# Optimization experiments

Hardware: AMD Instinct MI355X
Metric: run time of the kernel (lower is better)

Reference implementation:

```python
import jax, jax.numpy as jnp
import numpy as np

K = 5  # neighbors per node


def build_knn_adjacency(x, k=K):
    # x: (B, N, D) -> adj: (B, N, N)
    B, N, D = x.shape
    x_norm = x / jnp.clip(jnp.linalg.norm(x, axis=-1, keepdims=True), 1e-12)
    sim = jnp.einsum('bnd,bmd->bnm', x_norm, x_norm)  # (B, N, N)
    eye = jnp.eye(N, dtype=bool)
    sim = jnp.where(eye[None], jnp.asarray(-1.0, sim.dtype), sim)
    _, knn_idx = jax.lax.top_k(sim, k)  # (B, N, k)
    b_ix = jnp.arange(B)[:, None, None]
    i_ix = jnp.arange(N)[None, :, None]
    adj = jnp.zeros((B, N, N), dtype=x.dtype).at[b_ix, i_ix, knn_idx].set(1.0)
    adj = adj + jnp.eye(N, dtype=x.dtype)[None]
    return adj


def gcn_layer(x, adj, W, b):
    # deg-normalized aggregation then linear (torch Linear: x @ W.T + b)
    deg = adj.sum(axis=-1, keepdims=True)
    adj_norm = adj / jnp.clip(deg, 1.0)
    out = jnp.einsum('bnm,bmd->bnd', adj_norm, x)
    return out @ W.T + b


def setup_inputs() -> dict:
    key = jax.random.key(0)
    k1, k2, k3, k4, k5 = jax.random.split(key, 5)
    B, N, D, H = 32, 1024, 128, 128
    scale = 1.0 / np.sqrt(D)
    return {
        'x': jax.random.normal(k1, (B, N, D), dtype=jnp.float32),
        'W1': jax.random.normal(k2, (H, D), dtype=jnp.float32) * scale,
        'b1': jax.random.normal(k3, (H,), dtype=jnp.float32) * 0.01,
        'W2': jax.random.normal(k4, (H, H), dtype=jnp.float32) * scale,
        'b2': jax.random.normal(k5, (H,), dtype=jnp.float32) * 0.01,
    }


def reference(x, W1, b1, W2, b2):
    adj = build_knn_adjacency(x, k=K)
    h = x + jax.nn.relu(gcn_layer(x, adj, W1, b1))
    h = h + jax.nn.relu(gcn_layer(h, adj, W2, b2))
    return h  # pool='none' -> (B, N, hidden_dim)
```

## Files before the change

kernel.cpp:

```cpp
#include <hip/hip_runtime.h>
#include <float.h>
#include <math.h>

#define BB 32
#define NN 1024
#define DD 128
#define KK 5

typedef __attribute__((ext_vector_type(8))) short bf16x8;
typedef __attribute__((ext_vector_type(4))) float f32x4;

__device__ __forceinline__ unsigned short f2bf(float f) {
    unsigned int u = __float_as_uint(f);
    return (unsigned short)((u + 0x7FFFu + ((u >> 16) & 1u)) >> 16);
}
__device__ __forceinline__ float bf2f(unsigned short h) {
    return __uint_as_float(((unsigned int)h) << 16);
}

__device__ __forceinline__ void split2(const float4& a0, const float4& a1,
                                       bf16x8& hi, bf16x8& lo) {
    float v[8] = {a0.x, a0.y, a0.z, a0.w, a1.x, a1.y, a1.z, a1.w};
#pragma unroll
    for (int j = 0; j < 8; ++j) {
        unsigned short hb = f2bf(v[j]);
        float r = v[j] - bf2f(hb);
        unsigned short mb = f2bf(r);
        hi[j] = (short)hb;
        lo[j] = (short)mb;
    }
}

__global__ __launch_bounds__(256) void k_norm(const float* __restrict__ x,
                                              unsigned short* __restrict__ ph,
                                              unsigned short* __restrict__ pm,
                                              unsigned short* __restrict__ pl) {
    int row  = blockIdx.x * 4 + (threadIdx.x >> 6);
    int lane = threadIdx.x & 63;
    float2 v = *reinterpret_cast<const float2*>(x + (size_t)row * DD + lane * 2);
    float ss = v.x * v.x + v.y * v.y;
#pragma unroll
    for (int o = 32; o >= 1; o >>= 1) ss += __shfl_xor(ss, o);
    float inv = 1.0f / fmaxf(sqrtf(ss), 1e-12f);
    float y0 = v.x * inv, y1 = v.y * inv;

    unsigned short h0 = f2bf(y0);             float r0 = y0 - bf2f(h0);
    unsigned short m0 = f2bf(r0);             float s0 = r0 - bf2f(m0);
    unsigned short l0 = f2bf(s0);
    unsigned short h1 = f2bf(y1);             float r1 = y1 - bf2f(h1);
    unsigned short m1 = f2bf(r1);             float s1 = r1 - bf2f(m1);
    unsigned short l1 = f2bf(s1);

    size_t o = (size_t)row * DD + lane * 2;
    *reinterpret_cast<unsigned int*>(ph + o) = (unsigned int)h0 | ((unsigned int)h1 << 16);
    *reinterpret_cast<unsigned int*>(pm + o) = (unsigned int)m0 | ((unsigned int)m1 << 16);
    *reinterpret_cast<unsigned int*>(pl + o) = (unsigned int)l0 | ((unsigned int)l1 << 16);
}

union SMem {
    struct {
        unsigned short Ah[128][40], Am[128][40], Al[128][40];
        unsigned short Bh[128][40], Bm[128][40], Bl[128][40];
    } s;
    float q[4][32][68];
};

__device__ __forceinline__ void stage_plane(const unsigned short* __restrict__ g,
                                            unsigned short (*s)[40], int tid,
                                            size_t rowbase, int c) {
#pragma unroll
    for (int hh = 0; hh < 2; ++hh) {
        int u = tid + (hh << 8);
        int row = u >> 2, qq = u & 3;
        const float4 v = *reinterpret_cast<const float4*>(
            g + (rowbase + row) * DD + (c << 5) + (qq << 3));
        *reinterpret_cast<float4*>(&s[row][qq << 3]) = v;
    }
}

__global__ __launch_bounds__(256, 2) void k_sim(const unsigned short* __restrict__ ph,
                                                const unsigned short* __restrict__ pm,
                                                const unsigned short* __restrict__ pl,
                                                float* __restrict__ sim) {
    int bid = blockIdx.x;
    int lb  = (bid & 7) * 144 + (bid >> 3);
    int bl  = lb / 36;
    int p   = lb - bl * 36;
    int ti = 0;
    while (p >= 8 - ti) { p -= 8 - ti; ++ti; }
    int tj = ti + p;
    int R  = ti << 7, Cc = tj << 7;

    __shared__ SMem sm;

    int tid  = threadIdx.x;
    int wv   = tid >> 6;
    int lane = tid & 63;
    int wr = (wv >> 1) << 6;
    int wc = (wv & 1) << 6;
    int lg = lane >> 4, fr = lane & 15;

    size_t base = (size_t)bl * NN;
    size_t rbA = base + R, rbB = base + Cc;

    f32x4 acc[4][4];
#pragma unroll
    for (int i = 0; i < 4; ++i)
#pragma unroll
        for (int j = 0; j < 4; ++j) acc[i][j] = (f32x4){0.f, 0.f, 0.f, 0.f};

    int kk = lg << 3;

    for (int c = 0; c < 4; ++c) {
        if (c) __syncthreads();
        stage_plane(ph, sm.s.Ah, tid, rbA, c);
        stage_plane(pm, sm.s.Am, tid, rbA, c);
        stage_plane(pl, sm.s.Al, tid, rbA, c);
        stage_plane(ph, sm.s.Bh, tid, rbB, c);
        stage_plane(pm, sm.s.Bm, tid, rbB, c);
        stage_plane(pl, sm.s.Bl, tid, rbB, c);
        __syncthreads();

        bf16x8 bh[4], bm[4], blo[4];
#pragma unroll
        for (int cp = 0; cp < 4; ++cp) {
            int rb = wc + cp * 16 + fr;
            bh[cp]  = *reinterpret_cast<const bf16x8*>(&sm.s.Bh[rb][kk]);
            bm[cp]  = *reinterpret_cast<const bf16x8*>(&sm.s.Bm[rb][kk]);
            blo[cp] = *reinterpret_cast<const bf16x8*>(&sm.s.Bl[rb][kk]);
        }
#pragma unroll
        for (int rp = 0; rp < 4; ++rp) {
            int ra = wr + rp * 16 + fr;
            bf16x8 ah = *reinterpret_cast<const bf16x8*>(&sm.s.Ah[ra][kk]);
            bf16x8 am = *reinterpret_cast<const bf16x8*>(&sm.s.Am[ra][kk]);
            bf16x8 al = *reinterpret_cast<const bf16x8*>(&sm.s.Al[ra][kk]);
#pragma unroll
            for (int cp = 0; cp < 4; ++cp) {
                f32x4 cacc = acc[rp][cp];
                cacc = __builtin_amdgcn_mfma_f32_16x16x32_bf16(ah, bh[cp],  cacc, 0, 0, 0);
                cacc = __builtin_amdgcn_mfma_f32_16x16x32_bf16(ah, bm[cp],  cacc, 0, 0, 0);
                cacc = __builtin_amdgcn_mfma_f32_16x16x32_bf16(am, bh[cp],  cacc, 0, 0, 0);
                cacc = __builtin_amdgcn_mfma_f32_16x16x32_bf16(ah, blo[cp], cacc, 0, 0, 0);
                cacc = __builtin_amdgcn_mfma_f32_16x16x32_bf16(al, bh[cp],  cacc, 0, 0, 0);
                cacc = __builtin_amdgcn_mfma_f32_16x16x32_bf16(am, bm[cp],  cacc, 0, 0, 0);
                acc[rp][cp] = cacc;
            }
        }
    }

    __syncthreads();
    float (*q)[68] = sm.q[wv];
    float* Cb = sim + base * NN;

    if (ti != tj) {
#pragma unroll
        for (int hp = 0; hp < 2; ++hp) {
#pragma unroll
            for (int rp = 0; rp < 4; ++rp)
#pragma unroll
                for (int cpl = 0; cpl < 2; ++cpl) {
                    const f32x4 a = acc[rp][2 * hp + cpl];
                    *reinterpret_cast<float4*>(&q[cpl * 16 + fr][rp * 16 + lg * 4]) =
                        make_float4(a[0], a[1], a[2], a[3]);
                }
#pragma unroll
            for (int it = 0; it < 8; ++it) {
                int lcol = lg + 4 * it;
                const float4 v = *reinterpret_cast<const float4*>(&q[lcol][fr * 4]);
                *reinterpret_cast<float4*>(
                    &Cb[(size_t)(Cc + wc + 32 * hp + lcol) * NN + R + wr + fr * 4]) = v;
            }
        }
    }
#pragma unroll
    for (int hr = 0; hr < 2; ++hr) {
#pragma unroll
        for (int rpl = 0; rpl < 2; ++rpl)
#pragma unroll
            for (int cp = 0; cp < 4; ++cp)
#pragma unroll
                for (int reg = 0; reg < 4; ++reg)
                    q[rpl * 16 + lg * 4 + reg][cp * 16 + fr] = acc[2 * hr + rpl][cp][reg];
#pragma unroll
        for (int it = 0; it < 8; ++it) {
            int lrow = lg + 4 * it;
            const float4 v = *reinterpret_cast<const float4*>(&q[lrow][fr * 4]);
            *reinterpret_cast<float4*>(
                &Cb[(size_t)(R + wr + 32 * hr + lrow) * NN + Cc + wc + fr * 4]) = v;
        }
    }
}

__global__ __launch_bounds__(256) void k_topk(const float* __restrict__ sim,
                                              int* __restrict__ idx) {
    int lrow = blockIdx.x * 4 + (threadIdx.x >> 6);
    int lane = threadIdx.x & 63;
    const float* sr = sim + (size_t)lrow * NN;
    int i = lrow & (NN - 1);

    float v[16];
#pragma unroll
    for (int q = 0; q < 4; ++q) {
        float4 f = *reinterpret_cast<const float4*>(sr + lane * 16 + q * 4);
        v[q * 4 + 0] = f.x; v[q * 4 + 1] = f.y; v[q * 4 + 2] = f.z; v[q * 4 + 3] = f.w;
    }
    if ((i >> 4) == lane) {
        int s = i & 15;
#pragma unroll
        for (int j = 0; j < 16; ++j) if (j == s) v[j] = -FLT_MAX;
    }
    int* op = idx + (size_t)lrow * KK;
#pragma unroll
    for (int t = 0; t < KK; ++t) {
        float bv = v[0]; int bj = 0;
#pragma unroll
        for (int j = 1; j < 16; ++j) if (v[j] > bv) { bv = v[j]; bj = j; }
        int bm = (lane << 4) + bj;
#pragma unroll
        for (int o = 1; o < 64; o <<= 1) {
            float ov = __shfl_xor(bv, o);
            int   om = __shfl_xor(bm, o);
            if (ov > bv || (ov == bv && om < bm)) { bv = ov; bm = om; }
        }
        if ((bm >> 4) == lane) {
            int s = bm & 15;
#pragma unroll
            for (int j = 0; j < 16; ++j) if (j == s) v[j] = -FLT_MAX;
        }
        if (lane == 0) op[t] = bm;
    }
}

__global__ __launch_bounds__(256, 3) void k_gcn(const float* __restrict__ h,
                                                const int* __restrict__ idx,
                                                const float* __restrict__ W,
                                                const float* __restrict__ bias,
                                                const float* __restrict__ res,
                                                float* __restrict__ out) {
    int rt = blockIdx.x << 6;
    __shared__ float As[64][132];
    int tid = threadIdx.x;

    {
        int row = tid >> 2, fq = tid & 3;
        int grow = rt + row;
        const int* ip = idx + (size_t)grow * KK;
        const float* hb = h + (((size_t)grow >> 10) << 10) * DD;
        const float* hs = h + (size_t)grow * DD;
        int n0 = ip[0], n1 = ip[1], n2 = ip[2], n3 = ip[3], n4 = ip[4];
        const float* p0 = hb + (size_t)n0 * DD;
        const float* p1 = hb + (size_t)n1 * DD;
        const float* p2 = hb + (size_t)n2 * DD;
        const float* p3 = hb + (size_t)n3 * DD;
        const float* p4 = hb + (size_t)n4 * DD;
        const float cc = 1.0f / 6.0f;
#pragma unroll
        for (int rep = 0; rep < 8; ++rep) {
            int c = rep * 16 + fq * 4;
            float4 v  = *reinterpret_cast<const float4*>(hs + c);
            float4 u0 = *reinterpret_cast<const float4*>(p0 + c);
            float4 u1 = *reinterpret_cast<const float4*>(p1 + c);
            float4 u2 = *reinterpret_cast<const float4*>(p2 + c);
            float4 u3 = *reinterpret_cast<const float4*>(p3 + c);
            float4 u4 = *reinterpret_cast<const float4*>(p4 + c);
            v.x = (v.x + u0.x + u1.x + u2.x + u3.x + u4.x) * cc;
            v.y = (v.y + u0.y + u1.y + u2.y + u3.y + u4.y) * cc;
            v.z = (v.z + u0.z + u1.z + u2.z + u3.z + u4.z) * cc;
            v.w = (v.w + u0.w + u1.w + u2.w + u3.w + u4.w) * cc;
            *reinterpret_cast<float4*>(&As[row][c]) = v;
        }
    }
    __syncthreads();

    int wv   = tid >> 6;
    int lane = tid & 63;
    int wr = (wv >> 1) << 5;
    int wc = (wv & 1) << 6;
    int lg = lane >> 4, fr = lane & 15;

    f32x4 acc[2][4];
#pragma unroll
    for (int i = 0; i < 2; ++i)
#pragma unroll
        for (int j = 0; j < 4; ++j) acc[i][j] = (f32x4){0.f, 0.f, 0.f, 0.f};

#pragma unroll
    for (int kc = 0; kc < 4; ++kc) {
        int k0 = kc * 32 + lg * 8;
        bf16x8 ahh[2], ahm[2];
#pragma unroll
        for (int rp = 0; rp < 2; ++rp) {
            const float* ap = &As[wr + rp * 16 + fr][k0];
            split2(*reinterpret_cast<const float4*>(ap),
                   *reinterpret_cast<const float4*>(ap + 4), ahh[rp], ahm[rp]);
        }
        bf16x8 bhh[4], bhm[4];
#pragma unroll
        for (int cp = 0; cp < 4; ++cp) {
            const float* wp = W + (size_t)(wc + cp * 16 + fr) * DD + k0;
            split2(*reinterpret_cast<const float4*>(wp),
                   *reinterpret_cast<const float4*>(wp + 4), bhh[cp], bhm[cp]);
        }
#pragma unroll
        for (int rp = 0; rp < 2; ++rp)
#pragma unroll
            for (int cp = 0; cp < 4; ++cp) {
                f32x4 c = acc[rp][cp];
                c = __builtin_amdgcn_mfma_f32_16x16x32_bf16(ahh[rp], bhh[cp], c, 0, 0, 0);
                c = __builtin_amdgcn_mfma_f32_16x16x32_bf16(ahh[rp], bhm[cp], c, 0, 0, 0);
                c = __builtin_amdgcn_mfma_f32_16x16x32_bf16(ahm[rp], bhh[cp], c, 0, 0, 0);
                acc[rp][cp] = c;
            }
    }

    __syncthreads();
#pragma unroll
    for (int rp = 0; rp < 2; ++rp)
#pragma unroll
        for (int cp = 0; cp < 4; ++cp)
#pragma unroll
            for (int reg = 0; reg < 4; ++reg)
                As[wr + rp * 16 + lg * 4 + reg][wc + cp * 16 + fr] = acc[rp][cp][reg];
    __syncthreads();

#pragma unroll
    for (int rep = 0; rep < 8; ++rep) {
        int slot = tid + rep * 256;
        int row  = slot >> 5;
        int c4   = (slot & 31) << 2;
        float4 v  = *reinterpret_cast<const float4*>(&As[row][c4]);
        size_t go = (size_t)(rt + row) * DD + c4;
        const float4 r  = *reinterpret_cast<const float4*>(res + go);
        const float4 bz = *reinterpret_cast<const float4*>(bias + c4);
        float4 o;
        o.x = r.x + fmaxf(v.x + bz.x, 0.f);
        o.y = r.y + fmaxf(v.y + bz.y, 0.f);
        o.z = r.z + fmaxf(v.z + bz.z, 0.f);
        o.w = r.w + fmaxf(v.w + bz.w, 0.f);
        *reinterpret_cast<float4*>(out + go) = o;
    }
}

extern "C" void kernel_launch(void* const* d_in, const int* in_sizes, int n_in,
                              void* d_out, int out_size, void* d_ws, size_t ws_size,
                              hipStream_t stream) {
    const float* x  = (const float*)d_in[0];
    const float* W1 = (const float*)d_in[1];
    const float* b1 = (const float*)d_in[2];
    const float* W2 = (const float*)d_in[3];
    const float* b2 = (const float*)d_in[4];
    float* out = (float*)d_out;

    char* ws = (char*)d_ws;
    size_t pl_b  = (size_t)BB * NN * DD * 2;
    size_t h1_b  = (size_t)BB * NN * DD * 4;
    size_t idx_b = (size_t)BB * NN * KK * 4;
    unsigned short* ph = (unsigned short*)ws;  ws += pl_b;
    unsigned short* pm = (unsigned short*)ws;  ws += pl_b;
    unsigned short* pl = (unsigned short*)ws;  ws += pl_b;
    float* h1  = (float*)ws;                   ws += h1_b;
    int*   idx = (int*)ws;                     ws += idx_b;
    float* sim = (float*)ws;

    k_norm<<<BB * NN / 4, 256, 0, stream>>>(x, ph, pm, pl);
    k_sim<<<BB * 36, 256, 0, stream>>>(ph, pm, pl, sim);
    k_topk<<<BB * NN / 4, 256, 0, stream>>>(sim, idx);
    k_gcn<<<BB * NN / 64, 256, 0, stream>>>(x,  idx, W1, b1, x,  h1);
    k_gcn<<<BB * NN / 64, 256, 0, stream>>>(h1, idx, W2, b2, h1, out);
}
```

Baseline: 142.5 us.

## Halve GCN row tile, swizzle block order, and pad sim staging buffer

The GCN kernel now processes 32 rows per block instead of 64, doubling the grid to 1024 blocks so more of the GPU's compute units have work. Block indices are remapped so consecutive blocks land in different batches, spreading the neighbor gathers. The sim kernel's transpose staging buffer gets an odd row pitch (69) to reduce LDS bank conflicts. In exchange, each block reuses the W weight loads and their bf16 split over half as many rows, so weight traffic grows, and the occupancy hint drops to 2.

```diff
diff --git a/kernel.cpp b/kernel.cpp
--- a/kernel.cpp
+++ b/kernel.cpp
@@ -62,7 +62,7 @@
         unsigned short Ah[128][40], Am[128][40], Al[128][40];
         unsigned short Bh[128][40], Bm[128][40], Bl[128][40];
     } s;
-    float q[4][32][68];
+    float q[4][32][69];
 };
 
 __device__ __forceinline__ void stage_plane(const unsigned short* __restrict__ g,
@@ -150,7 +150,7 @@
     }
 
     __syncthreads();
-    float (*q)[68] = sm.q[wv];
+    float (*q)[69] = sm.q[wv];
     float* Cb = sim + base * NN;
 
     if (ti != tj) {
@@ -232,18 +232,19 @@
     }
 }
 
-__global__ __launch_bounds__(256, 3) void k_gcn(const float* __restrict__ h,
+__global__ __launch_bounds__(256, 2) void k_gcn(const float* __restrict__ h,
                                                 const int* __restrict__ idx,
                                                 const float* __restrict__ W,
                                                 const float* __restrict__ bias,
                                                 const float* __restrict__ res,
                                                 float* __restrict__ out) {
-    int rt = blockIdx.x << 6;
-    __shared__ float As[64][132];
+    int lb = (blockIdx.x & 7) * 128 + (blockIdx.x >> 3);
+    int rt = lb << 5;
+    __shared__ float As[32][132];
     int tid = threadIdx.x;
 
     {
-        int row = tid >> 2, fq = tid & 3;
+        int row = tid >> 3, sub = tid & 7;
         int grow = rt + row;
         const int* ip = idx + (size_t)grow * KK;
         const float* hb = h + (((size_t)grow >> 10) << 10) * DD;
@@ -256,8 +257,8 @@
         const float* p4 = hb + (size_t)n4 * DD;
         const float cc = 1.0f / 6.0f;
 #pragma unroll
-        for (int rep = 0; rep < 8; ++rep) {
-            int c = rep * 16 + fq * 4;
+        for (int qq = 0; qq < 4; ++qq) {
+            int c = sub * 16 + qq * 4;
             float4 v  = *reinterpret_cast<const float4*>(hs + c);
             float4 u0 = *reinterpret_cast<const float4*>(p0 + c);
             float4 u1 = *reinterpret_cast<const float4*>(p1 + c);
@@ -275,25 +276,22 @@
 
     int wv   = tid >> 6;
     int lane = tid & 63;
-    int wr = (wv >> 1) << 5;
+    int wr = (wv >> 1) << 4;
     int wc = (wv & 1) << 6;
     int lg = lane >> 4, fr = lane & 15;
 
-    f32x4 acc[2][4];
-#pragma unroll
-    for (int i = 0; i < 2; ++i)
-#pragma unroll
-        for (int j = 0; j < 4; ++j) acc[i][j] = (f32x4){0.f, 0.f, 0.f, 0.f};
+    f32x4 acc[4];
+#pragma unroll
+    for (int j = 0; j < 4; ++j) acc[j] = (f32x4){0.f, 0.f, 0.f, 0.f};
 
 #pragma unroll
     for (int kc = 0; kc < 4; ++kc) {
         int k0 = kc * 32 + lg * 8;
-        bf16x8 ahh[2], ahm[2];
-#pragma unroll
-        for (int rp = 0; rp < 2; ++rp) {
-            const float* ap = &As[wr + rp * 16 + fr][k0];
+        bf16x8 ahh, ahm;
+        {
+            const float* ap = &As[wr + fr][k0];
             split2(*reinterpret_cast<const float4*>(ap),
-                   *reinterpret_cast<const float4*>(ap + 4), ahh[rp], ahm[rp]);
+                   *reinterpret_cast<const float4*>(ap + 4), ahh, ahm);
         }
         bf16x8 bhh[4], bhm[4];
 #pragma unroll
@@ -303,29 +301,25 @@
                    *reinterpret_cast<const float4*>(wp + 4), bhh[cp], bhm[cp]);
         }
 #pragma unroll
-        for (int rp = 0; rp < 2; ++rp)
-#pragma unroll
-            for (int cp = 0; cp < 4; ++cp) {
-                f32x4 c = acc[rp][cp];
-                c = __builtin_amdgcn_mfma_f32_16x16x32_bf16(ahh[rp], bhh[cp], c, 0, 0, 0);
-                c = __builtin_amdgcn_mfma_f32_16x16x32_bf16(ahh[rp], bhm[cp], c, 0, 0, 0);
-                c = __builtin_amdgcn_mfma_f32_16x16x32_bf16(ahm[rp], bhh[cp], c, 0, 0, 0);
-                acc[rp][cp] = c;
-            }
+        for (int cp = 0; cp < 4; ++cp) {
+            f32x4 c = acc[cp];
+            c = __builtin_amdgcn_mfma_f32_16x16x32_bf16(ahh, bhh[cp], c, 0, 0, 0);
+            c = __builtin_amdgcn_mfma_f32_16x16x32_bf16(ahh, bhm[cp], c, 0, 0, 0);
+            c = __builtin_amdgcn_mfma_f32_16x16x32_bf16(ahm, bhh[cp], c, 0, 0, 0);
+            acc[cp] = c;
+        }
     }
 
     __syncthreads();
 #pragma unroll
-    for (int rp = 0; rp < 2; ++rp)
-#pragma unroll
-        for (int cp = 0; cp < 4; ++cp)
-#pragma unroll
-            for (int reg = 0; reg < 4; ++reg)
-                As[wr + rp * 16 + lg * 4 + reg][wc + cp * 16 + fr] = acc[rp][cp][reg];
+    for (int cp = 0; cp < 4; ++cp)
+#pragma unroll
+        for (int reg = 0; reg < 4; ++reg)
+            As[wr + lg * 4 + reg][wc + cp * 16 + fr] = acc[cp][reg];
     __syncthreads();
 
 #pragma unroll
-    for (int rep = 0; rep < 8; ++rep) {
+    for (int rep = 0; rep < 4; ++rep) {
         int slot = tid + rep * 256;
         int row  = slot >> 5;
         int c4   = (slot & 31) << 2;
@@ -366,6 +360,6 @@
     k_norm<<<BB * NN / 4, 256, 0, stream>>>(x, ph, pm, pl);
     k_sim<<<BB * 36, 256, 0, stream>>>(ph, pm, pl, sim);
     k_topk<<<BB * NN / 4, 256, 0, stream>>>(sim, idx);
-    k_gcn<<<BB * NN / 64, 256, 0, stream>>>(x,  idx, W1, b1, x,  h1);
-    k_gcn<<<BB * NN / 64, 256, 0, stream>>>(h1, idx, W2, b2, h1, out);
-}
+    k_gcn<<<BB * NN / 32, 256, 0, stream>>>(x,  idx, W1, b1, x,  h1);
+    k_gcn<<<BB * NN / 32, 256, 0, stream>>>(h1, idx, W2, b2, h1, out);
+}
```

Result: slower. 165.9 us (+16.5%).

## Prune top-k scan using per-segment row maxima emitted by the similarity kernel

Applied to the files above, without the earlier changes.

The similarity kernel's epilogue now records, for each row, the maximum over each of 16 column segments of 64 entries. It writes these for both the tile and its mirrored transpose, with the diagonal masked. The top-k kernel first picks a threshold equal to the 5th-largest segment maximum and rescans only the segments that can hold a winner. It merges the candidates with a packed 64-bit key insertion network and a wave-wide reduction. This avoids reading each full 4 KB row of the similarity matrix. The cost is extra shuffle/reduction work and small scattered stores in the similarity kernel, plus a data-dependent loop in top-k.

```diff
diff --git a/kernel.cpp b/kernel.cpp
--- a/kernel.cpp
+++ b/kernel.cpp
@@ -9,6 +9,7 @@
 
 typedef __attribute__((ext_vector_type(8))) short bf16x8;
 typedef __attribute__((ext_vector_type(4))) float f32x4;
+typedef unsigned long long ull;
 
 __device__ __forceinline__ unsigned short f2bf(float f) {
     unsigned int u = __float_as_uint(f);
@@ -16,6 +17,21 @@
 }
 __device__ __forceinline__ float bf2f(unsigned short h) {
     return __uint_as_float(((unsigned int)h) << 16);
+}
+
+__device__ __forceinline__ ull mkkey(float v, int col) {
+    unsigned int u = __float_as_uint(v);
+    unsigned int ou = u ^ (unsigned)((((int)u) >> 31) | 0x80000000);
+    return ((ull)ou << 32) | (unsigned)(1023 - col);
+}
+
+__device__ __forceinline__ void ins5(ull k, ull* s) {
+    bool b0 = k > s[0], b1 = k > s[1], b2 = k > s[2], b3 = k > s[3], b4 = k > s[4];
+    s[4] = b4 ? (b3 ? s[3] : k) : s[4];
+    s[3] = b3 ? (b2 ? s[2] : k) : s[3];
+    s[2] = b2 ? (b1 ? s[1] : k) : s[2];
+    s[1] = b1 ? (b0 ? s[0] : k) : s[1];
+    s[0] = b0 ? k : s[0];
 }
 
 __device__ __forceinline__ void split2(const float4& a0, const float4& a1,
@@ -81,7 +97,8 @@
 __global__ __launch_bounds__(256, 2) void k_sim(const unsigned short* __restrict__ ph,
                                                 const unsigned short* __restrict__ pm,
                                                 const unsigned short* __restrict__ pl,
-                                                float* __restrict__ sim) {
+                                                float* __restrict__ sim,
+                                                float* __restrict__ smx) {
     int bid = blockIdx.x;
     int lb  = (bid & 7) * 144 + (bid >> 3);
     int bl  = lb / 36;
@@ -149,6 +166,46 @@
         }
     }
 
+    {
+        int slotR = 2 * tj + (wc >> 6);
+#pragma unroll
+        for (int rp = 0; rp < 4; ++rp)
+#pragma unroll
+            for (int reg = 0; reg < 4; ++reg) {
+                int grow = R + wr + rp * 16 + lg * 4 + reg;
+                float v0 = acc[rp][0][reg], v1 = acc[rp][1][reg];
+                float v2 = acc[rp][2][reg], v3 = acc[rp][3][reg];
+                if (ti == tj) {
+                    int c0 = Cc + wc + fr;
+                    v0 = (c0      == grow) ? -FLT_MAX : v0;
+                    v1 = (c0 + 16 == grow) ? -FLT_MAX : v1;
+                    v2 = (c0 + 32 == grow) ? -FLT_MAX : v2;
+                    v3 = (c0 + 48 == grow) ? -FLT_MAX : v3;
+                }
+                float m = fmaxf(fmaxf(v0, v1), fmaxf(v2, v3));
+#pragma unroll
+                for (int o = 1; o < 16; o <<= 1) m = fmaxf(m, __shfl_xor(m, o));
+                if (fr == 0) smx[(base + grow) * 16 + slotR] = m;
+            }
+        if (ti != tj) {
+            int slotM = 2 * ti + (wr >> 6);
+#pragma unroll
+            for (int cp = 0; cp < 4; ++cp) {
+                float m = -FLT_MAX;
+#pragma unroll
+                for (int rp = 0; rp < 4; ++rp)
+#pragma unroll
+                    for (int reg = 0; reg < 4; ++reg) m = fmaxf(m, acc[rp][cp][reg]);
+                m = fmaxf(m, __shfl_xor(m, 16));
+                m = fmaxf(m, __shfl_xor(m, 32));
+                if (lg == 0) {
+                    int node = Cc + wc + cp * 16 + fr;
+                    smx[(base + node) * 16 + slotM] = m;
+                }
+            }
+        }
+    }
+
     __syncthreads();
     float (*q)[68] = sm.q[wv];
     float* Cb = sim + base * NN;
@@ -193,42 +250,52 @@
 }
 
 __global__ __launch_bounds__(256) void k_topk(const float* __restrict__ sim,
+                                              const float* __restrict__ smx,
                                               int* __restrict__ idx) {
-    int lrow = blockIdx.x * 4 + (threadIdx.x >> 6);
+    int row  = blockIdx.x * 4 + (threadIdx.x >> 6);
     int lane = threadIdx.x & 63;
-    const float* sr = sim + (size_t)lrow * NN;
-    int i = lrow & (NN - 1);
-
-    float v[16];
-#pragma unroll
-    for (int q = 0; q < 4; ++q) {
-        float4 f = *reinterpret_cast<const float4*>(sr + lane * 16 + q * 4);
-        v[q * 4 + 0] = f.x; v[q * 4 + 1] = f.y; v[q * 4 + 2] = f.z; v[q * 4 + 3] = f.w;
-    }
-    if ((i >> 4) == lane) {
-        int s = i & 15;
-#pragma unroll
-        for (int j = 0; j < 16; ++j) if (j == s) v[j] = -FLT_MAX;
-    }
-    int* op = idx + (size_t)lrow * KK;
-#pragma unroll
-    for (int t = 0; t < KK; ++t) {
-        float bv = v[0]; int bj = 0;
-#pragma unroll
-        for (int j = 1; j < 16; ++j) if (v[j] > bv) { bv = v[j]; bj = j; }
-        int bm = (lane << 4) + bj;
+    const float* sr = sim + (size_t)row * NN;
+    int i = row & (NN - 1);
+
+    float morig = (lane < 16) ? smx[(size_t)row * 16 + lane] : -FLT_MAX;
+    float m = morig, tau = morig;
+#pragma unroll
+    for (int t = 0; t < 5; ++t) {
+        float bv = m; int bs = lane;
 #pragma unroll
         for (int o = 1; o < 64; o <<= 1) {
             float ov = __shfl_xor(bv, o);
-            int   om = __shfl_xor(bm, o);
-            if (ov > bv || (ov == bv && om < bm)) { bv = ov; bm = om; }
-        }
-        if ((bm >> 4) == lane) {
-            int s = bm & 15;
-#pragma unroll
-            for (int j = 0; j < 16; ++j) if (j == s) v[j] = -FLT_MAX;
-        }
-        if (lane == 0) op[t] = bm;
+            int   os = __shfl_xor(bs, o);
+            if (ov > bv || (ov == bv && os < bs)) { bv = ov; bs = os; }
+        }
+        tau = bv;
+        if (lane == bs) m = -FLT_MAX;
+    }
+    unsigned long long sel = __ballot(lane < 16 && morig >= tau);
+
+    ull keys[5] = {0, 0, 0, 0, 0};
+    while (sel) {
+        int s = __ffsll(sel) - 1;
+        sel &= sel - 1;
+        int col = s * 64 + lane;
+        float v = sr[col];
+        if (col == i) v = -FLT_MAX;
+        ins5(mkkey(v, col), keys);
+    }
+
+    int* op = idx + (size_t)row * KK;
+    ull k0 = keys[0], k1 = keys[1], k2 = keys[2], k3 = keys[3], k4 = keys[4];
+#pragma unroll
+    for (int t = 0; t < 5; ++t) {
+        ull w = k0;
+#pragma unroll
+        for (int o = 1; o < 64; o <<= 1) {
+            ull x = __shfl_xor(w, o); if (x > w) w = x;
+        }
+        if (lane == t) op[t] = 1023 - (int)(w & 0xFFFFFFFFu);
+        bool adv = (k0 == w);
+        k0 = adv ? k1 : k0; k1 = adv ? k2 : k1;
+        k2 = adv ? k3 : k2; k3 = adv ? k4 : k3; k4 = adv ? 0ULL : k4;
     }
 }
 
@@ -356,16 +423,18 @@
     size_t pl_b  = (size_t)BB * NN * DD * 2;
     size_t h1_b  = (size_t)BB * NN * DD * 4;
     size_t idx_b = (size_t)BB * NN * KK * 4;
+    size_t smx_b = (size_t)BB * NN * 16 * 4;
     unsigned short* ph = (unsigned short*)ws;  ws += pl_b;
     unsigned short* pm = (unsigned short*)ws;  ws += pl_b;
     unsigned short* pl = (unsigned short*)ws;  ws += pl_b;
     float* h1  = (float*)ws;                   ws += h1_b;
     int*   idx = (int*)ws;                     ws += idx_b;
+    float* smx = (float*)ws;                   ws += smx_b;
     float* sim = (float*)ws;
 
     k_norm<<<BB * NN / 4, 256, 0, stream>>>(x, ph, pm, pl);
-    k_sim<<<BB * 36, 256, 0, stream>>>(ph, pm, pl, sim);
-    k_topk<<<BB * NN / 4, 256, 0, stream>>>(sim, idx);
+    k_sim<<<BB * 36, 256, 0, stream>>>(ph, pm, pl, sim, smx);
+    k_topk<<<BB * NN / 4, 256, 0, stream>>>(sim, smx, idx);
     k_gcn<<<BB * NN / 64, 256, 0, stream>>>(x,  idx, W1, b1, x,  h1);
     k_gcn<<<BB * NN / 64, 256, 0, stream>>>(h1, idx, W2, b2, h1, out);
 }
```

Result: slower. 194.3 us (+36.4%).
